# Performance work log

Measured on AMD Instinct MI355X. Metric: run time of the kernel, lower is better.

## Reference

```python
import jax, jax.numpy as jnp
import numpy as np

LEVELS = 5          # perfect binary tree depth
N_NODES = 2**LEVELS - 1  # 31, level-order: children of p are 2p+1, 2p+2
V, E, ENC, H, LBL = 50000, 128, 128, 128, 104
B, L = 64, 128


def setup_inputs() -> dict:
    key = jax.random.key(0)
    ks = jax.random.split(key, 16)
    g = lambda k, shape: (jax.random.normal(k, shape, dtype=jnp.float32) * 0.02)
    return {
        "tokens": jax.random.randint(ks[0], (B, L, N_NODES), 0, V),
        "embedding": g(ks[1], (V, E)),
        "Wc_w": g(ks[2], (ENC, E)),
        "Wc_b": g(ks[3], (ENC,)),
        "Wih_f": g(ks[4], (3 * H, ENC)),
        "Whh_f": g(ks[5], (3 * H, H)),
        "bih_f": g(ks[6], (3 * H,)),
        "bhh_f": g(ks[7], (3 * H,)),
        "Wih_b": g(ks[8], (3 * H, ENC)),
        "Whh_b": g(ks[9], (3 * H, H)),
        "bih_b": g(ks[10], (3 * H,)),
        "bhh_b": g(ks[11], (3 * H,)),
        "Wout": g(ks[12], (LBL, 2 * H)),
        "bout": g(ks[13], (LBL,)),
    }


def _tree_encode(tokens, embedding, Wc_w, Wc_b):
    # node encoding h(n) = W_c(emb(tok_n)) + sum(children h); statement enc = max over nodes
    x = embedding[tokens]                       # [B, L, N, E] gather
    h = jnp.einsum("blne,ce->blnc", x, Wc_w) + Wc_b  # [B, L, N, ENC]
    for lvl in reversed(range(LEVELS - 1)):     # bottom-up accumulation
        s = 2**lvl - 1
        n = 2**lvl
        cs = 2 * s + 1                          # first child index of this level
        left = h[..., cs:cs + 2 * n:2, :]
        right = h[..., cs + 1:cs + 2 * n:2, :]
        h = h.at[..., s:s + n, :].add(left + right)
    # node_list max across all recursion calls == max over all tree nodes
    return jnp.max(h, axis=2)                   # [B, L, ENC]


def _gru_dir(xs, Wih, Whh, bih, bhh, reverse):
    # xs: [B, L, ENC]; PyTorch GRU cell equations, h0 = 0
    gi = jnp.einsum("blc,gc->blg", xs, Wih) + bih  # precompute input gates [B, L, 3H]
    h0 = jnp.zeros((xs.shape[0], H), dtype=xs.dtype)

    def step(h, gi_t):
        gh = h @ Whh.T + bhh
        ir, iz, inn = jnp.split(gi_t, 3, axis=-1)
        hr, hz, hn = jnp.split(gh, 3, axis=-1)
        r = jax.nn.sigmoid(ir + hr)
        z = jax.nn.sigmoid(iz + hz)
        n = jnp.tanh(inn + r * hn)
        h_new = (1.0 - z) * n + z * h
        return h_new, h_new

    _, ys = jax.lax.scan(step, h0, gi.transpose(1, 0, 2), reverse=reverse)
    return ys.transpose(1, 0, 2)                # [B, L, H]


def reference(tokens, embedding, Wc_w, Wc_b,
              Wih_f, Whh_f, bih_f, bhh_f,
              Wih_b, Whh_b, bih_b, bhh_b,
              Wout, bout):
    encodes = _tree_encode(tokens, embedding, Wc_w, Wc_b)   # [B, L, ENC]
    fwd = _gru_dir(encodes, Wih_f, Whh_f, bih_f, bhh_f, reverse=False)
    bwd = _gru_dir(encodes, Wih_b, Whh_b, bih_b, bhh_b, reverse=True)
    gru_out = jnp.concatenate([fwd, bwd], axis=-1)          # [B, L, 2H]
    pooled = jnp.max(gru_out, axis=1)                       # max_pool1d over time
    return pooled @ Wout.T + bout                           # [B, LBL]
```

## Files before the change

kernel.cpp:

```cpp
#include <hip/hip_runtime.h>
#include <hip/hip_bf16.h>
#include <math.h>

#define NN   31
#define VV   50000
#define EE   128
#define HH   128
#define BB   64
#define LL   128
#define NLBL 104

template <bool BIAS>
__global__ __launch_bounds__(256, 2) void gemm128(const float* __restrict__ A,
                                                  const float* __restrict__ Bm,
                                                  const float* __restrict__ bias,
                                                  float* __restrict__ C,
                                                  int M, int N) {
    __shared__ float4 As[64 * 17];
    __shared__ float4 Bs[128 * 17];
    const int tid = threadIdx.x;
    const int m0 = blockIdx.x * 64;
    const int n0 = blockIdx.y * 128;
    const float4* Af4 = (const float4*)A;
    const float4* Bf4 = (const float4*)Bm;

    const int r0 = (tid >> 4) * 4;
    const int cb = tid & 15;
    float acc[4][8] = {};

    for (int kk = 0; kk < 2; ++kk) {
        for (int f = tid; f < 128 * 16; f += 256) {
            int r = f >> 4, e = f & 15;
            Bs[r * 17 + e] = Bf4[(size_t)(n0 + r) * 32 + kk * 16 + e];
        }
        for (int f = tid; f < 64 * 16; f += 256) {
            int r = f >> 4, e = f & 15;
            float4 v = make_float4(0.f, 0.f, 0.f, 0.f);
            if (m0 + r < M) v = Af4[(size_t)(m0 + r) * 32 + kk * 16 + e];
            As[r * 17 + e] = v;
        }
        __syncthreads();
        #pragma unroll
        for (int e = 0; e < 16; ++e) {
            float4 a[4], b[8];
            #pragma unroll
            for (int i = 0; i < 4; ++i) a[i] = As[(r0 + i) * 17 + e];
            #pragma unroll
            for (int j = 0; j < 8; ++j) b[j] = Bs[(cb + j * 16) * 17 + e];
            #pragma unroll
            for (int i = 0; i < 4; ++i) {
                #pragma unroll
                for (int j = 0; j < 8; ++j) {
                    acc[i][j] += a[i].x * b[j].x;
                    acc[i][j] += a[i].y * b[j].y;
                    acc[i][j] += a[i].z * b[j].z;
                    acc[i][j] += a[i].w * b[j].w;
                }
            }
        }
        __syncthreads();
    }

    #pragma unroll
    for (int i = 0; i < 4; ++i) {
        int row = m0 + r0 + i;
        if (row < M) {
            #pragma unroll
            for (int j = 0; j < 8; ++j) {
                int col = n0 + cb + j * 16;
                float v = acc[i][j];
                if (BIAS) v += bias[col];
                C[(size_t)row * N + col] = v;
            }
        }
    }
}

__global__ __launch_bounds__(256) void tree_encode(const int* __restrict__ tok,
                                                   const float* __restrict__ Wemb,
                                                   const float* __restrict__ Wcb,
                                                   float* __restrict__ enc) {
    __shared__ int st[2][NN];
    const int tid = threadIdx.x;
    const int p = tid >> 7;
    const int c = tid & 127;
    const int bl = blockIdx.x * 2;
    if (tid < 2 * NN) {
        int pp = tid / NN, jj = tid - pp * NN;
        st[pp][jj] = tok[(size_t)(bl + pp) * NN + jj];
    }
    __syncthreads();

    float v[NN];
    #pragma unroll
    for (int j = 0; j < NN; ++j)
        v[j] = Wemb[(size_t)st[p][j] * 128 + c];
    #pragma unroll
    for (int i = 14; i >= 0; --i)
        v[i] += v[2 * i + 1] + v[2 * i + 2];

    const float wb = Wcb[c];
    float m = v[0] + 31.f * wb;
    #pragma unroll
    for (int i = 1; i <= 2; ++i)  m = fmaxf(m, v[i] + 15.f * wb);
    #pragma unroll
    for (int i = 3; i <= 6; ++i)  m = fmaxf(m, v[i] + 7.f * wb);
    #pragma unroll
    for (int i = 7; i <= 14; ++i) m = fmaxf(m, v[i] + 3.f * wb);
    #pragma unroll
    for (int i = 15; i <= 30; ++i) m = fmaxf(m, v[i] + wb);

    enc[(size_t)(bl + p) * 128 + c] = m;
}

__device__ __forceinline__ float sigm(float x) { return 1.f / (1.f + __expf(-x)); }
__device__ __forceinline__ float tanh_f(float x) { return 1.f - 2.f / (1.f + __expf(2.f * x)); }

__global__ __launch_bounds__(384, 1) void gru_scan(const float* __restrict__ gi_f,
                                                   const float* __restrict__ gi_b,
                                                   const float* __restrict__ Whh_f,
                                                   const float* __restrict__ Whh_b,
                                                   const float* __restrict__ bhh_f,
                                                   const float* __restrict__ bhh_b,
                                                   float* __restrict__ pooled) {
    const int g = threadIdx.x;
    const int dir = blockIdx.x & 1;
    const int b = blockIdx.x >> 1;
    const float* gi  = dir ? gi_b  : gi_f;
    const float* Whh = dir ? Whh_b : Whh_f;
    const float* bhh = dir ? bhh_b : bhh_f;

    __shared__ __align__(16) float h[128];
    __shared__ float sz[128], shn[128], sinn[128];

    float4 w[32];
    const float4* wf4 = (const float4*)Whh;
    #pragma unroll
    for (int q = 0; q < 32; ++q) w[q] = wf4[(size_t)g * 32 + q];
    const float bh = bhh[g];
    if (g < 128) h[g] = 0.f;
    float m = -INFINITY;
    __syncthreads();

    const float4* hf4 = (const float4*)h;
    for (int s = 0; s < LL; ++s) {
        const int t = dir ? (LL - 1 - s) : s;
        const float gv = gi[((size_t)b * LL + t) * 384 + g];

        float acc = bh;
        #pragma unroll
        for (int q = 0; q < 32; ++q) {
            float4 hv = hf4[q];
            acc += w[q].x * hv.x + w[q].y * hv.y + w[q].z * hv.z + w[q].w * hv.w;
        }

        float r = 0.f, hold = 0.f;
        if (g < 128) {
            r = sigm(gv + acc);
            hold = h[g];
        } else if (g < 256) {
            sz[g - 128] = sigm(gv + acc);
        } else {
            shn[g - 256] = acc;
            sinn[g - 256] = gv;
        }
        __syncthreads();
        if (g < 128) {
            float n = tanh_f(sinn[g] + r * shn[g]);
            float z = sz[g];
            float hn = (1.f - z) * n + z * hold;
            h[g] = hn;
            m = fmaxf(m, hn);
        }
        __syncthreads();
    }
    if (g < 128) pooled[((size_t)b * 2 + dir) * 128 + g] = m;
}

__global__ __launch_bounds__(128) void out_head(const float* __restrict__ pooled,
                                                const float* __restrict__ Wout,
                                                const float* __restrict__ bout,
                                                float* __restrict__ out) {
    __shared__ __align__(16) float p[256];
    const int b = blockIdx.x, o = threadIdx.x;
    if (o < 64) ((float4*)p)[o] = ((const float4*)(pooled + (size_t)b * 256))[o];
    __syncthreads();
    if (o < NLBL) {
        float acc = bout[o];
        const float4* wf4 = (const float4*)(Wout + (size_t)o * 256);
        const float4* pf4 = (const float4*)p;
        #pragma unroll 8
        for (int q = 0; q < 64; ++q) {
            float4 wv = wf4[q], pv = pf4[q];
            acc += wv.x * pv.x + wv.y * pv.y + wv.z * pv.z + wv.w * pv.w;
        }
        out[(size_t)b * NLBL + o] = acc;
    }
}

extern "C" void kernel_launch(void* const* d_in, const int* in_sizes, int n_in,
                              void* d_out, int out_size, void* d_ws, size_t ws_size,
                              hipStream_t stream) {
    const int*   tokens = (const int*)  d_in[0];
    const float* emb    = (const float*)d_in[1];
    const float* Wc_w   = (const float*)d_in[2];
    const float* Wc_b   = (const float*)d_in[3];
    const float* Wih_f  = (const float*)d_in[4];
    const float* Whh_f  = (const float*)d_in[5];
    const float* bih_f  = (const float*)d_in[6];
    const float* bhh_f  = (const float*)d_in[7];
    const float* Wih_b  = (const float*)d_in[8];
    const float* Whh_b  = (const float*)d_in[9];
    const float* bih_b  = (const float*)d_in[10];
    const float* bhh_b  = (const float*)d_in[11];
    const float* Wout   = (const float*)d_in[12];
    const float* bout   = (const float*)d_in[13];
    float* out = (float*)d_out;
    float* ws  = (float*)d_ws;

    float* Wemb = ws;
    float* enc  = Wemb + (size_t)VV * 128;
    float* gi_f = enc  + (size_t)BB * LL * 128;
    float* gi_b = gi_f + (size_t)BB * LL * 384;
    float* pool = gi_b + (size_t)BB * LL * 384;

    gemm128<false><<<dim3(782, 1), 256, 0, stream>>>(emb, Wc_w, nullptr, Wemb, VV, 128);
    tree_encode<<<dim3(4096), 256, 0, stream>>>(tokens, Wemb, Wc_b, enc);
    gemm128<true><<<dim3(128, 3), 256, 0, stream>>>(enc, Wih_f, bih_f, gi_f, BB * LL, 384);
    gemm128<true><<<dim3(128, 3), 256, 0, stream>>>(enc, Wih_b, bih_b, gi_b, BB * LL, 384);
    gru_scan<<<dim3(128), 384, 0, stream>>>(gi_f, gi_b, Whh_f, Whh_b, bhh_f, bhh_b, pool);
    out_head<<<dim3(64), 128, 0, stream>>>(pool, Wout, bout, out);
}
```

Before: 325.1 us.

## Restructure GRU scan with quad-split dot products and single barrier per step

The GRU recurrence kernel now splits each hidden unit's three gate dot products across four lanes, each covering a quarter of the K dimension, and reduces them with DPP cross-lane adds. Each lane pair computes r, z and n locally, so the shared gate scratch arrays and one of the two barriers per step go away. The hidden state is double-buffered in shared memory and the next step's input-gate values are prefetched. Separately, the forward and backward input-projection GEMMs are merged into one launch using blockIdx.z. Half the threads sit idle during the gate math, and the DPP reductions add some per-step latency.

```diff
diff --git a/kernel.cpp b/kernel.cpp
--- a/kernel.cpp
+++ b/kernel.cpp
@@ -12,10 +12,17 @@
 
 template <bool BIAS>
 __global__ __launch_bounds__(256, 2) void gemm128(const float* __restrict__ A,
-                                                  const float* __restrict__ Bm,
-                                                  const float* __restrict__ bias,
-                                                  float* __restrict__ C,
+                                                  const float* __restrict__ B0,
+                                                  const float* __restrict__ B1,
+                                                  const float* __restrict__ bias0,
+                                                  const float* __restrict__ bias1,
+                                                  float* __restrict__ C0,
+                                                  float* __restrict__ C1,
                                                   int M, int N) {
+    const float* Bm  = blockIdx.z ? B1 : B0;
+    const float* bias = blockIdx.z ? bias1 : bias0;
+    float* C = blockIdx.z ? C1 : C0;
+
     __shared__ float4 As[64 * 17];
     __shared__ float4 Bs[128 * 17];
     const int tid = threadIdx.x;
@@ -116,79 +123,115 @@
 __device__ __forceinline__ float sigm(float x) { return 1.f / (1.f + __expf(-x)); }
 __device__ __forceinline__ float tanh_f(float x) { return 1.f - 2.f / (1.f + __expf(2.f * x)); }
 
-__global__ __launch_bounds__(384, 1) void gru_scan(const float* __restrict__ gi_f,
+__device__ __forceinline__ float dpp_xor1(float x) {
+    return __builtin_bit_cast(float,
+        __builtin_amdgcn_mov_dpp(__builtin_bit_cast(int, x), 0xB1, 0xF, 0xF, true));
+}
+__device__ __forceinline__ float dpp_xor2(float x) {
+    return __builtin_bit_cast(float,
+        __builtin_amdgcn_mov_dpp(__builtin_bit_cast(int, x), 0x4E, 0xF, 0xF, true));
+}
+__device__ __forceinline__ float quad_sum(float x) {
+    x += dpp_xor1(x);
+    x += dpp_xor2(x);
+    return x;
+}
+
+__global__ __launch_bounds__(256, 1) void gru_scan(const float* __restrict__ gi_f,
                                                    const float* __restrict__ gi_b,
                                                    const float* __restrict__ Whh_f,
                                                    const float* __restrict__ Whh_b,
                                                    const float* __restrict__ bhh_f,
                                                    const float* __restrict__ bhh_b,
                                                    float* __restrict__ pooled) {
-    const int g = threadIdx.x;
+    const int tid = threadIdx.x;
+    const int g   = tid >> 2;
+    const int p   = tid & 3;
     const int dir = blockIdx.x & 1;
-    const int b = blockIdx.x >> 1;
+    const int b   = blockIdx.x >> 1;
     const float* gi  = dir ? gi_b  : gi_f;
     const float* Whh = dir ? Whh_b : Whh_f;
     const float* bhh = dir ? bhh_b : bhh_f;
 
-    __shared__ __align__(16) float h[128];
-    __shared__ float sz[128], shn[128], sinn[128];
-
-    float4 w[32];
+    __shared__ __align__(16) float hbuf[2][128];
+
+    float4 w[6][8];
     const float4* wf4 = (const float4*)Whh;
     #pragma unroll
-    for (int q = 0; q < 32; ++q) w[q] = wf4[(size_t)g * 32 + q];
-    const float bh = bhh[g];
-    if (g < 128) h[g] = 0.f;
-    float m = -INFINITY;
+    for (int r6 = 0; r6 < 6; ++r6)
+        #pragma unroll
+        for (int q = 0; q < 8; ++q)
+            w[r6][q] = wf4[(size_t)(r6 * 64 + g) * 32 + p * 8 + q];
+
+    const int c = g + p * 64;
+    float bh_r = 0.f, bh_z = 0.f, bh_n = 0.f;
+    if (p < 2) { bh_r = bhh[c]; bh_z = bhh[128 + c]; bh_n = bhh[256 + c]; }
+
+    float hold = 0.f, m = -INFINITY;
+    if (tid < 128) { hbuf[0][tid] = 0.f; }
+
+    float gr = 0.f, gz = 0.f, gn = 0.f;
+    {
+        const int t0 = dir ? (LL - 1) : 0;
+        const float* grow = gi + ((size_t)b * LL + t0) * 384;
+        if (p < 2) { gr = grow[c]; gz = grow[128 + c]; gn = grow[256 + c]; }
+    }
     __syncthreads();
 
-    const float4* hf4 = (const float4*)h;
     for (int s = 0; s < LL; ++s) {
-        const int t = dir ? (LL - 1 - s) : s;
-        const float gv = gi[((size_t)b * LL + t) * 384 + g];
-
-        float acc = bh;
+        const int cur = s & 1;
+        float gr_n = 0.f, gz_n = 0.f, gn_n = 0.f;
+        if (p < 2 && s + 1 < LL) {
+            const int t1 = dir ? (LL - 2 - s) : (s + 1);
+            const float* grow = gi + ((size_t)b * LL + t1) * 384;
+            gr_n = grow[c]; gz_n = grow[128 + c]; gn_n = grow[256 + c];
+        }
+
+        const float4* hq = ((const float4*)hbuf[cur]) + p * 8;
+        float a0 = 0.f, a1 = 0.f, a2 = 0.f, a3 = 0.f, a4 = 0.f, a5 = 0.f;
         #pragma unroll
-        for (int q = 0; q < 32; ++q) {
-            float4 hv = hf4[q];
-            acc += w[q].x * hv.x + w[q].y * hv.y + w[q].z * hv.z + w[q].w * hv.w;
-        }
-
-        float r = 0.f, hold = 0.f;
-        if (g < 128) {
-            r = sigm(gv + acc);
-            hold = h[g];
-        } else if (g < 256) {
-            sz[g - 128] = sigm(gv + acc);
-        } else {
-            shn[g - 256] = acc;
-            sinn[g - 256] = gv;
-        }
+        for (int q = 0; q < 8; ++q) {
+            const float4 hv = hq[q];
+            a0 += w[0][q].x * hv.x + w[0][q].y * hv.y + w[0][q].z * hv.z + w[0][q].w * hv.w;
+            a1 += w[1][q].x * hv.x + w[1][q].y * hv.y + w[1][q].z * hv.z + w[1][q].w * hv.w;
+            a2 += w[2][q].x * hv.x + w[2][q].y * hv.y + w[2][q].z * hv.z + w[2][q].w * hv.w;
+            a3 += w[3][q].x * hv.x + w[3][q].y * hv.y + w[3][q].z * hv.z + w[3][q].w * hv.w;
+            a4 += w[4][q].x * hv.x + w[4][q].y * hv.y + w[4][q].z * hv.z + w[4][q].w * hv.w;
+            a5 += w[5][q].x * hv.x + w[5][q].y * hv.y + w[5][q].z * hv.z + w[5][q].w * hv.w;
+        }
+        a0 = quad_sum(a0); a1 = quad_sum(a1); a2 = quad_sum(a2);
+        a3 = quad_sum(a3); a4 = quad_sum(a4); a5 = quad_sum(a5);
+
+        if (p < 2) {
+            const float ghr = (p ? a1 : a0) + bh_r;
+            const float ghz = (p ? a3 : a2) + bh_z;
+            const float ghn = (p ? a5 : a4) + bh_n;
+            const float r = sigm(gr + ghr);
+            const float z = sigm(gz + ghz);
+            const float n = tanh_f(gn + r * ghn);
+            const float hn = (1.f - z) * n + z * hold;
+            hold = hn;
+            m = fmaxf(m, hn);
+            hbuf[cur ^ 1][c] = hn;
+        }
+        gr = gr_n; gz = gz_n; gn = gn_n;
         __syncthreads();
-        if (g < 128) {
-            float n = tanh_f(sinn[g] + r * shn[g]);
-            float z = sz[g];
-            float hn = (1.f - z) * n + z * hold;
-            h[g] = hn;
-            m = fmaxf(m, hn);
-        }
-        __syncthreads();
-    }
-    if (g < 128) pooled[((size_t)b * 2 + dir) * 128 + g] = m;
+    }
+    if (p < 2) pooled[((size_t)b * 2 + dir) * 128 + c] = m;
 }
 
 __global__ __launch_bounds__(128) void out_head(const float* __restrict__ pooled,
                                                 const float* __restrict__ Wout,
                                                 const float* __restrict__ bout,
                                                 float* __restrict__ out) {
-    __shared__ __align__(16) float p[256];
+    __shared__ __align__(16) float pbuf[256];
     const int b = blockIdx.x, o = threadIdx.x;
-    if (o < 64) ((float4*)p)[o] = ((const float4*)(pooled + (size_t)b * 256))[o];
+    if (o < 64) ((float4*)pbuf)[o] = ((const float4*)(pooled + (size_t)b * 256))[o];
     __syncthreads();
     if (o < NLBL) {
         float acc = bout[o];
         const float4* wf4 = (const float4*)(Wout + (size_t)o * 256);
-        const float4* pf4 = (const float4*)p;
+        const float4* pf4 = (const float4*)pbuf;
         #pragma unroll 8
         for (int q = 0; q < 64; ++q) {
             float4 wv = wf4[q], pv = pf4[q];
@@ -224,10 +267,11 @@
     float* gi_b = gi_f + (size_t)BB * LL * 384;
     float* pool = gi_b + (size_t)BB * LL * 384;
 
-    gemm128<false><<<dim3(782, 1), 256, 0, stream>>>(emb, Wc_w, nullptr, Wemb, VV, 128);
+    gemm128<false><<<dim3(782, 1, 1), 256, 0, stream>>>(
+        emb, Wc_w, Wc_w, nullptr, nullptr, Wemb, Wemb, VV, 128);
     tree_encode<<<dim3(4096), 256, 0, stream>>>(tokens, Wemb, Wc_b, enc);
-    gemm128<true><<<dim3(128, 3), 256, 0, stream>>>(enc, Wih_f, bih_f, gi_f, BB * LL, 384);
-    gemm128<true><<<dim3(128, 3), 256, 0, stream>>>(enc, Wih_b, bih_b, gi_b, BB * LL, 384);
-    gru_scan<<<dim3(128), 384, 0, stream>>>(gi_f, gi_b, Whh_f, Whh_b, bhh_f, bhh_b, pool);
+    gemm128<true><<<dim3(128, 3, 2), 256, 0, stream>>>(
+        enc, Wih_f, Wih_b, bih_f, bih_b, gi_f, gi_b, BB * LL, 384);
+    gru_scan<<<dim3(128), 256, 0, stream>>>(gi_f, gi_b, Whh_f, Whh_b, bhh_f, bhh_b, pool);
     out_head<<<dim3(64), 128, 0, stream>>>(pool, Wout, bout, out);
 }
```

Result: faster. 295.2 us (-9.2%).
